# Performance work log

Measured on AMD Instinct MI355X. Metric: run time of the kernel, lower is better.

## Reference

```python
import jax, jax.numpy as jnp
import numpy as np

B, S, K_IN = 8, 2048, 512
D_MODEL = 1024
N_INPUT = 2048
N_PROCESS = 4096
HIDDEN = 4096  # default hidden_dim = n_input * 2
K = 256


def setup_inputs() -> dict:
    key = jax.random.key(0)
    ks = jax.random.split(key, 7)
    return {
        "selected_activations": jax.random.normal(ks[0], (B, S, K_IN), dtype=jnp.float32),
        "selected_indices": jax.random.randint(ks[1], (B, K_IN), 0, N_INPUT),
        "k": K,
        "combination_weights": jax.random.normal(ks[2], (N_PROCESS, N_INPUT), dtype=jnp.float32) * np.float32(np.sqrt(2.0 / N_INPUT)),
        "output_projections": jax.random.normal(ks[3], (N_PROCESS, D_MODEL), dtype=jnp.float32) * np.float32(np.sqrt(2.0 / N_PROCESS)),
        "w1": jax.random.normal(ks[4], (HIDDEN, N_INPUT), dtype=jnp.float32) * np.float32(np.sqrt(2.0 / (N_INPUT + HIDDEN))),
        "b1": jnp.zeros((HIDDEN,), dtype=jnp.float32),
        "w2": jax.random.normal(ks[5], (N_PROCESS, HIDDEN), dtype=jnp.float32) * np.float32(np.sqrt(2.0 / (HIDDEN + N_PROCESS))),
        "b2": jnp.zeros((N_PROCESS,), dtype=jnp.float32),
    }


def reference(selected_activations, selected_indices, k, combination_weights,
              output_projections, w1, b1, w2, b2):
    bsz = selected_indices.shape[0]
    n_input = combination_weights.shape[1]

    # Per-batch gather of combination weights: [B, k_in, n_process]
    sel_w = combination_weights.T[selected_indices]

    # Process activations: [B, S, n_process], exact (erf) GELU like torch F.gelu
    process_activations = jax.nn.gelu(
        jnp.einsum('bsk,bkp->bsp', selected_activations, sel_w), approximate=False)

    # One-hot style input-selection mask via scatter: [B, n_input]
    input_selection = jnp.zeros((bsz, n_input), dtype=jnp.float32)
    input_selection = input_selection.at[jnp.arange(bsz)[:, None], selected_indices].set(1.0)

    # Combination analyzer MLP: Linear -> GELU -> Linear
    h = jax.nn.gelu(input_selection @ w1.T + b1, approximate=False)
    combination_relevance = h @ w2.T + b2  # [B, n_process]

    # Router scores and top-k process selection
    activation_scores = process_activations.max(axis=1)  # [B, n_process]
    final_scores = activation_scores * jax.nn.sigmoid(combination_relevance)
    _, process_indices = jax.lax.top_k(final_scores, k)  # [B, k]

    # Gather selected process activations [B, S, k] and projections [B, k, d_model]
    sel_pa = jnp.take_along_axis(process_activations, process_indices[:, None, :], axis=2)
    sel_proj = output_projections[process_indices]

    # Final projection: [B, S, d_model]
    return jnp.einsum('bsk,bkd->bsd', sel_pa, sel_proj)
```

## Files before the change

### kernel.cpp

```cpp
#include <hip/hip_runtime.h>
#include <math.h>

#define B 8
#define S 2048
#define KIN 512
#define NIN 2048
#define NP 4096
#define HID 4096
#define DM 1024
#define TOPK 256

typedef __bf16 bf16x8 __attribute__((ext_vector_type(8)));
typedef __bf16 bf16x4 __attribute__((ext_vector_type(4)));
typedef float f32x4 __attribute__((ext_vector_type(4)));

__device__ __forceinline__ float gelu_exact(float x) {
    return 0.5f * x * (1.0f + erff(x * 0.70710678118654752440f));
}

__device__ __forceinline__ void atomicMaxFloat(float* addr, float val) {
    if (val >= 0.0f) atomicMax((int*)addr, __float_as_int(val));
    else             atomicMin((unsigned int*)addr, __float_as_uint(val));
}

__device__ __forceinline__ void async_copy16(void* lds, const void* g) {
    __builtin_amdgcn_global_load_lds(
        (__attribute__((address_space(1))) void*)g,
        (__attribute__((address_space(3))) void*)lds, 16, 0, 0);
}

__global__ __launch_bounds__(256) void init_kernel(float* scores, float* relacc,
                                                   float* hacc, unsigned* maskb,
                                                   int* selcnt) {
    int t = blockIdx.x * blockDim.x + threadIdx.x;
    if (t < B * NP)  { scores[t] = __int_as_float(0xFF800000); relacc[t] = 0.f; }
    if (t < B * HID) hacc[t] = 0.f;
    if (t < NIN)     maskb[t] = 0u;
    if (t < B)       selcnt[t] = 0;
}

__global__ __launch_bounds__(256) void scatter_maskbits(const int* __restrict__ idx,
                                                        unsigned* __restrict__ maskb) {
    int t = blockIdx.x * blockDim.x + threadIdx.x;
    if (t >= B * KIN) return;
    int b = t / KIN;
    atomicOr(&maskb[idx[t]], 1u << b);
}

__global__ __launch_bounds__(256) void pack_A(const float* __restrict__ A,
                                              __bf16* __restrict__ Apack) {
    size_t t = (size_t)blockIdx.x * 256 + threadIdx.x;
    size_t f = t * 4;
    size_t rowi = f >> 9;
    int j = (int)(f & 511);
    float4 v = *(const float4*)(A + f);
    __bf16 h0 = (__bf16)v.x, h1 = (__bf16)v.y, h2 = (__bf16)v.z, h3 = (__bf16)v.w;
    bf16x4 hv = {h0, h1, h2, h3};
    bf16x4 lv = {(__bf16)(v.x - (float)h0), (__bf16)(v.y - (float)h1),
                 (__bf16)(v.z - (float)h2), (__bf16)(v.w - (float)h3)};
    __bf16* orow = Apack + rowi * 1024;
    *(bf16x4*)(orow + j) = hv;
    *(bf16x4*)(orow + 512 + j) = lv;
}

__global__ __launch_bounds__(256) void gather_pack_w(const float* __restrict__ cw,
                                                     const int* __restrict__ idx,
                                                     __bf16* __restrict__ wpack) {
    __shared__ float rowbuf[4][NIN];
    __shared__ int sidx[B][KIN];
    int p0 = blockIdx.x * 4;
    int tid = threadIdx.x;
    for (int t = tid; t < B * KIN; t += 256) sidx[t >> 9][t & 511] = idx[t];
#pragma unroll
    for (int r = 0; r < 4; ++r)
        for (int c = tid; c < NIN / 4; c += 256)
            *(float4*)&rowbuf[r][c * 4] = *(const float4*)&cw[(size_t)(p0 + r) * NIN + c * 4];
    __syncthreads();
#pragma unroll
    for (int r = 0; r < 4; ++r) {
        int p = p0 + r;
        for (int b = 0; b < B; ++b) {
            __bf16* orow = wpack + ((size_t)b * NP + p) * 1024;
            for (int j = tid; j < KIN; j += 256) {
                float x = rowbuf[r][sidx[b][j]];
                __bf16 hh = (__bf16)x;
                orow[j] = hh;
                orow[512 + j] = (__bf16)(x - (float)hh);
            }
        }
    }
}

template <int EPI, int NSEG, int KSEG, int LDA, int LDB, int BROWS, int LDOUT>
__global__ __launch_bounds__(256) void mfma_gemm(const __bf16* __restrict__ Ap,
                                                 const __bf16* __restrict__ Bp,
                                                 void* __restrict__ outp) {
    __shared__ __align__(16) __bf16 As[128 * 64];
    __shared__ __align__(16) __bf16 Ws[128 * 64];
    const int b = blockIdx.z;
    const int s0 = blockIdx.x * 128;
    const int p0 = blockIdx.y * 128;
    const int tid = threadIdx.x;
    const int w = tid >> 6, lane = tid & 63;
    const int wr = w >> 1, wc = w & 1;
    const int ldRow = lane >> 3;
    const int ldCol = ((lane & 7) ^ (ldRow & 7)) * 8;
    const int fr = lane & 15;
    const int fq = lane >> 4;
    const __bf16* Ab = Ap + ((size_t)b * S + s0) * LDA;
    const __bf16* Bb = Bp + ((size_t)b * BROWS + p0) * LDB;

    f32x4 acc[4][4] = {};

    for (int seg = 0; seg < NSEG; ++seg) {
        const int aoff = (seg == 1) ? KSEG : 0;
        const int boff = (seg == 2) ? KSEG : 0;
        for (int k0 = 0; k0 < KSEG; k0 += 64) {
            __syncthreads();
#pragma unroll
            for (int i = 0; i < 4; ++i) {
                const __bf16* g = Ab + (size_t)(w * 32 + i * 8 + ldRow) * LDA + aoff + k0 + ldCol;
                async_copy16(&As[(w * 32 + i * 8) * 64], g);
            }
#pragma unroll
            for (int i = 0; i < 4; ++i) {
                const __bf16* g = Bb + (size_t)(w * 32 + i * 8 + ldRow) * LDB + boff + k0 + ldCol;
                async_copy16(&Ws[(w * 32 + i * 8) * 64], g);
            }
            __syncthreads();
#pragma unroll
            for (int ks = 0; ks < 2; ++ks) {
                bf16x8 af[4], bfr[4];
#pragma unroll
                for (int i = 0; i < 4; ++i) {
                    int R = wr * 64 + i * 16 + fr;
                    af[i] = *(const bf16x8*)&As[R * 64 + (((ks * 4 + fq) ^ (R & 7)) * 8)];
                }
#pragma unroll
                for (int j = 0; j < 4; ++j) {
                    int R = wc * 64 + j * 16 + fr;
                    bfr[j] = *(const bf16x8*)&Ws[R * 64 + (((ks * 4 + fq) ^ (R & 7)) * 8)];
                }
#pragma unroll
                for (int i = 0; i < 4; ++i)
#pragma unroll
                    for (int j = 0; j < 4; ++j)
                        acc[i][j] = __builtin_amdgcn_mfma_f32_16x16x32_bf16(af[i], bfr[j], acc[i][j], 0, 0, 0);
            }
        }
    }

    if constexpr (EPI == 1) {
        __bf16* o = (__bf16*)outp;
#pragma unroll
        for (int i = 0; i < 4; ++i)
#pragma unroll
            for (int r = 0; r < 4; ++r) {
                size_t row = (size_t)b * S + s0 + wr * 64 + i * 16 + fq * 4 + r;
#pragma unroll
                for (int j = 0; j < 4; ++j)
                    o[row * LDOUT + p0 + wc * 64 + j * 16 + fr] = (__bf16)gelu_exact(acc[i][j][r]);
            }
    } else {
        float* o = (float*)outp;
#pragma unroll
        for (int i = 0; i < 4; ++i)
#pragma unroll
            for (int r = 0; r < 4; ++r) {
                size_t row = (size_t)b * S + s0 + wr * 64 + i * 16 + fq * 4 + r;
#pragma unroll
                for (int j = 0; j < 4; ++j)
                    o[row * LDOUT + p0 + wc * 64 + j * 16 + fr] = acc[i][j][r];
            }
    }
}

__device__ __forceinline__ void stage64(__bf16* ldsTile, const __bf16* gRow0,
                                        int rbase, int ldg, int koff, int w, int lane) {
    const int rr = lane >> 3;
    const int gc = ((lane & 7) ^ rr) * 8;
    const __bf16* g = gRow0 + (size_t)(rbase + w * 8 + rr) * ldg + (koff + gc);
    async_copy16(ldsTile + (rbase + w * 8) * 64, g);
}

template <int EPI, int NSEG, int KSEG, int LDA, int LDB, int BROWS, int LDOUT>
__global__ __launch_bounds__(512, 2) void mfma_gemm256(const __bf16* __restrict__ Ap,
                                                       const __bf16* __restrict__ Bp,
                                                       void* __restrict__ outp) {
    constexpr int TPS = KSEG / 64;
    constexpr int NT = NSEG * TPS;
    __shared__ __align__(16) __bf16 As[2][256 * 64];
    __shared__ __align__(16) __bf16 Ws[2][256 * 64];

    const int flat = blockIdx.x + (blockIdx.y << 3) + (blockIdx.z << 7);
    const int b = flat & 7;
    const int j = flat >> 3;
    const int s0 = (j & 7) * 256;
    const int p0 = (j >> 3) * 256;

    const int tid = threadIdx.x;
    const int w = tid >> 6, lane = tid & 63;
    const int wr = w >> 2, wc = w & 3;
    const int fr = lane & 15, fq = lane >> 4;
    const __bf16* Ab = Ap + ((size_t)b * S + s0) * LDA;
    const __bf16* Bb = Bp + ((size_t)b * BROWS + p0) * LDB;

    auto offs = [&](int t, int& ao, int& bo) {
        int seg = t / TPS, k0 = (t % TPS) * 64;
        ao = ((NSEG == 3 && seg == 1) ? KSEG : 0) + k0;
        bo = ((NSEG == 3 && seg == 2) ? KSEG : 0) + k0;
    };

    int offA[2][2][4];
    int offB[2][4];
#pragma unroll
    for (int kk = 0; kk < 2; ++kk) {
#pragma unroll
        for (int mh = 0; mh < 2; ++mh)
#pragma unroll
            for (int mi = 0; mi < 4; ++mi) {
                int R = wr * 128 + mh * 64 + mi * 16 + fr;
                offA[kk][mh][mi] = R * 64 + (((kk * 4 + fq) ^ (R & 7)) * 8);
            }
#pragma unroll
        for (int nj = 0; nj < 4; ++nj) {
            int R = wc * 64 + nj * 16 + fr;
            offB[kk][nj] = R * 64 + (((kk * 4 + fq) ^ (R & 7)) * 8);
        }
    }

    f32x4 acc[8][4] = {};

    {
        int ao, bo;
        offs(0, ao, bo);
        stage64(&As[0][0], Ab, 0, LDA, ao, w, lane);
        stage64(&As[0][0], Ab, 128, LDA, ao, w, lane);
        stage64(&As[0][0], Ab, 64, LDA, ao, w, lane);
        stage64(&As[0][0], Ab, 192, LDA, ao, w, lane);
        stage64(&Ws[0][0], Bb, 0, LDB, bo, w, lane);
        stage64(&Ws[0][0], Bb, 128, LDB, bo, w, lane);
        stage64(&Ws[0][0], Bb, 64, LDB, bo, w, lane);
        stage64(&Ws[0][0], Bb, 192, LDB, bo, w, lane);
        if (NT > 1) {
            offs(1, ao, bo);
            stage64(&As[1][0], Ab, 0, LDA, ao, w, lane);
            stage64(&As[1][0], Ab, 128, LDA, ao, w, lane);
            stage64(&Ws[1][0], Bb, 0, LDB, bo, w, lane);
            stage64(&Ws[1][0], Bb, 128, LDB, bo, w, lane);
            asm volatile("s_waitcnt vmcnt(4)");
        } else {
            asm volatile("s_waitcnt vmcnt(0)");
        }
        __builtin_amdgcn_s_barrier();
    }

    for (int t = 0; t < NT; ++t) {
        const __bf16* Asb = &As[t & 1][0];
        const __bf16* Wsb = &Ws[t & 1][0];
        __bf16* Asn = &As[(t & 1) ^ 1][0];
        __bf16* Wsn = &Ws[(t & 1) ^ 1][0];
        bf16x8 af[4], bfr[4];

#pragma unroll
        for (int i = 0; i < 4; ++i) af[i] = *(const bf16x8*)&Asb[offA[0][0][i]];
#pragma unroll
        for (int n = 0; n < 4; ++n) bfr[n] = *(const bf16x8*)&Wsb[offB[0][n]];
        if (t + 1 < NT) {
            int ao, bo;
            offs(t + 1, ao, bo);
            stage64(Asn, Ab, 64, LDA, ao, w, lane);
            stage64(Asn, Ab, 192, LDA, ao, w, lane);
            stage64(Wsn, Bb, 64, LDB, bo, w, lane);
            stage64(Wsn, Bb, 192, LDB, bo, w, lane);
        }
        __builtin_amdgcn_s_barrier();
        asm volatile("s_waitcnt lgkmcnt(0)");
        __builtin_amdgcn_s_setprio(1);
#pragma unroll
        for (int mi = 0; mi < 4; ++mi)
#pragma unroll
            for (int nj = 0; nj < 4; ++nj)
                acc[mi][nj] = __builtin_amdgcn_mfma_f32_16x16x32_bf16(af[mi], bfr[nj], acc[mi][nj], 0, 0, 0);
        __builtin_amdgcn_s_setprio(0);
        __builtin_amdgcn_s_barrier();

#pragma unroll
        for (int i = 0; i < 4; ++i) af[i] = *(const bf16x8*)&Asb[offA[0][1][i]];
        __builtin_amdgcn_s_barrier();
        asm volatile("s_waitcnt lgkmcnt(0)");
        __builtin_amdgcn_s_setprio(1);
#pragma unroll
        for (int mi = 0; mi < 4; ++mi)
#pragma unroll
            for (int nj = 0; nj < 4; ++nj)
                acc[4 + mi][nj] = __builtin_amdgcn_mfma_f32_16x16x32_bf16(af[mi], bfr[nj], acc[4 + mi][nj], 0, 0, 0);
        __builtin_amdgcn_s_setprio(0);
        __builtin_amdgcn_s_barrier();

#pragma unroll
        for (int i = 0; i < 4; ++i) af[i] = *(const bf16x8*)&Asb[offA[1][0][i]];
#pragma unroll
        for (int n = 0; n < 4; ++n) bfr[n] = *(const bf16x8*)&Wsb[offB[1][n]];
        __builtin_amdgcn_s_barrier();
        asm volatile("s_waitcnt lgkmcnt(0)");
        __builtin_amdgcn_s_setprio(1);
#pragma unroll
        for (int mi = 0; mi < 4; ++mi)
#pragma unroll
            for (int nj = 0; nj < 4; ++nj)
                acc[mi][nj] = __builtin_amdgcn_mfma_f32_16x16x32_bf16(af[mi], bfr[nj], acc[mi][nj], 0, 0, 0);
        __builtin_amdgcn_s_setprio(0);
        __builtin_amdgcn_s_barrier();

#pragma unroll
        for (int i = 0; i < 4; ++i) af[i] = *(const bf16x8*)&Asb[offA[1][1][i]];
        if (t + 2 < NT) {
            int ao, bo;
            offs(t + 2, ao, bo);
            stage64((__bf16*)Asb, Ab, 0, LDA, ao, w, lane);
            stage64((__bf16*)Asb, Ab, 128, LDA, ao, w, lane);
            stage64((__bf16*)Wsb, Bb, 0, LDB, bo, w, lane);
            stage64((__bf16*)Wsb, Bb, 128, LDB, bo, w, lane);
            asm volatile("s_waitcnt vmcnt(4)");
        } else {
            asm volatile("s_waitcnt vmcnt(0)");
        }
        __builtin_amdgcn_s_barrier();
        asm volatile("s_waitcnt lgkmcnt(0)");
        __builtin_amdgcn_s_setprio(1);
#pragma unroll
        for (int mi = 0; mi < 4; ++mi)
#pragma unroll
            for (int nj = 0; nj < 4; ++nj)
                acc[4 + mi][nj] = __builtin_amdgcn_mfma_f32_16x16x32_bf16(af[mi], bfr[nj], acc[4 + mi][nj], 0, 0, 0);
        __builtin_amdgcn_s_setprio(0);
        __builtin_amdgcn_s_barrier();
    }

    if constexpr (EPI == 0) {
        float* scores = (float*)outp;
#pragma unroll
        for (int nj = 0; nj < 4; ++nj) {
            float mx = -INFINITY, mn = INFINITY;
#pragma unroll
            for (int mi = 0; mi < 8; ++mi)
#pragma unroll
                for (int r = 0; r < 4; ++r) {
                    float v = acc[mi][nj][r];
                    mx = fmaxf(mx, v);
                    mn = fminf(mn, v);
                }
            mx = fmaxf(mx, __shfl_xor(mx, 16));
            mx = fmaxf(mx, __shfl_xor(mx, 32));
            mn = fminf(mn, __shfl_xor(mn, 16));
            mn = fminf(mn, __shfl_xor(mn, 32));
            if (fq == 0) {
                float m = fmaxf(gelu_exact(mx), gelu_exact(mn));
                atomicMaxFloat(&scores[(size_t)b * LDOUT + p0 + wc * 64 + nj * 16 + fr], m);
            }
        }
    } else if constexpr (EPI == 1) {
        __bf16* o = (__bf16*)outp;
#pragma unroll
        for (int mi = 0; mi < 8; ++mi)
#pragma unroll
            for (int r = 0; r < 4; ++r) {
                size_t row = (size_t)b * S + s0 + wr * 128 + mi * 16 + fq * 4 + r;
#pragma unroll
                for (int nj = 0; nj < 4; ++nj)
                    o[row * LDOUT + p0 + wc * 64 + nj * 16 + fr] = (__bf16)gelu_exact(acc[mi][nj][r]);
            }
    } else {
        float* o = (float*)outp;
#pragma unroll
        for (int mi = 0; mi < 8; ++mi)
#pragma unroll
            for (int r = 0; r < 4; ++r) {
                size_t row = (size_t)b * S + s0 + wr * 128 + mi * 16 + fq * 4 + r;
#pragma unroll
                for (int nj = 0; nj < 4; ++nj)
                    o[row * LDOUT + p0 + wc * 64 + nj * 16 + fr] = acc[mi][nj][r];
            }
    }
}

__global__ __launch_bounds__(256) void mlp1_part(const float* __restrict__ w1,
                                                 const unsigned* __restrict__ maskb,
                                                 float* __restrict__ hacc) {
    __shared__ unsigned smb[512];
    int i0 = blockIdx.x * 64;
    int c0 = blockIdx.y * 512;
    int tid = threadIdx.x;
    for (int c = tid; c < 512; c += 256) smb[c] = maskb[c0 + c];
    __syncthreads();
    int r = tid >> 2, cq = tid & 3;
    const float* row = w1 + (size_t)(i0 + r) * NIN + c0;
    float acc[B] = {};
    for (int it = 0; it < 32; ++it) {
        int c = it * 16 + cq * 4;
        float4 v = *(const float4*)(row + c);
        float vv[4] = {v.x, v.y, v.z, v.w};
#pragma unroll
        for (int e = 0; e < 4; ++e) {
            unsigned mb = smb[c + e];
#pragma unroll
            for (int bb = 0; bb < B; ++bb)
                if (mb & (1u << bb)) acc[bb] += vv[e];
        }
    }
#pragma unroll
    for (int bb = 0; bb < B; ++bb)
        atomicAdd(&hacc[bb * HID + i0 + r], acc[bb]);
}

__global__ __launch_bounds__(256) void fin1(const float* __restrict__ hacc,
                                            const float* __restrict__ b1,
                                            float* __restrict__ h) {
    int t = blockIdx.x * 256 + threadIdx.x;
    if (t < B * HID) h[t] = gelu_exact(hacc[t] + b1[t & (HID - 1)]);
}

__global__ __launch_bounds__(256) void mlp2_part(const float* __restrict__ w2,
                                                 const float* __restrict__ h,
                                                 float* __restrict__ relacc) {
    __shared__ float sh[B][512];
    int p0 = blockIdx.x * 64;
    int c0 = blockIdx.y * 512;
    int tid = threadIdx.x;
    for (int i = tid; i < B * 128; i += 256) {
        int bb = i >> 7, c4 = i & 127;
        *(float4*)&sh[bb][c4 * 4] = *(const float4*)&h[(size_t)bb * HID + c0 + c4 * 4];
    }
    __syncthreads();
    int r = tid >> 2, cq = tid & 3;
    const float* row = w2 + (size_t)(p0 + r) * HID + c0;
    float acc[B] = {};
    for (int it = 0; it < 32; ++it) {
        int c = it * 16 + cq * 4;
        float4 v = *(const float4*)(row + c);
#pragma unroll
        for (int bb = 0; bb < B; ++bb)
            acc[bb] += v.x * sh[bb][c] + v.y * sh[bb][c + 1] + v.z * sh[bb][c + 2] + v.w * sh[bb][c + 3];
    }
#pragma unroll
    for (int bb = 0; bb < B; ++bb)
        atomicAdd(&relacc[bb * NP + p0 + r], acc[bb]);
}

__global__ __launch_bounds__(256) void topk_select(const float* __restrict__ scores,
                                                   const float* __restrict__ relacc,
                                                   const float* __restrict__ b2,
                                                   int* __restrict__ selidx,
                                                   int* __restrict__ selcnt) {
    __shared__ float sc[NP];
    int b = blockIdx.y;
    int p = blockIdx.x * 256 + threadIdx.x;
    for (int c = threadIdx.x; c < NP; c += 256) {
        float rel = relacc[(size_t)b * NP + c] + b2[c];
        sc[c] = scores[(size_t)b * NP + c] * (1.0f / (1.0f + expf(-rel)));
    }
    __syncthreads();
    float my = sc[p];
    int cnt = 0;
    for (int q = 0; q < NP; ++q) {
        float v = sc[q];
        cnt += (v > my) || (v == my && q < p);
    }
    if (cnt < TOPK) {
        int pos = atomicAdd(&selcnt[b], 1);
        selidx[b * TOPK + pos] = p;
    }
}

__global__ __launch_bounds__(256) void wsel_gather(const __bf16* __restrict__ wpack,
                                                   const int* __restrict__ selidx,
                                                   __bf16* __restrict__ wsel) {
    int kk = blockIdx.x, b = blockIdx.y;
    int sel = selidx[b * TOPK + kk];
    const unsigned* src = (const unsigned*)(wpack + ((size_t)b * NP + sel) * 1024);
    unsigned* dst = (unsigned*)(wsel + ((size_t)b * TOPK + kk) * 512);
    dst[threadIdx.x] = src[threadIdx.x];
}

__global__ __launch_bounds__(256) void projT_gather(const float* __restrict__ proj,
                                                    const int* __restrict__ selidx,
                                                    __bf16* __restrict__ PT) {
    __shared__ float tile[64][68];
    __shared__ int sel[64];
    int b = blockIdx.z, d0 = blockIdx.x * 64, k0 = blockIdx.y * 64;
    int tid = threadIdx.x;
    if (tid < 64) sel[tid] = selidx[b * TOPK + k0 + tid];
    __syncthreads();
    for (int r = 0; r < 4; ++r) {
        int kk = r * 16 + (tid >> 4);
        float4 v = *(const float4*)&proj[(size_t)sel[kk] * DM + d0 + (tid & 15) * 4];
        *(float4*)&tile[kk][(tid & 15) * 4] = v;
    }
    __syncthreads();
    for (int r = 0; r < 16; ++r) {
        int dd = r * 4 + (tid >> 6);
        int kk = tid & 63;
        PT[((size_t)b * DM + d0 + dd) * TOPK + k0 + kk] = (__bf16)tile[kk][dd];
    }
}

extern "C" void kernel_launch(void* const* d_in, const int* in_sizes, int n_in,
                              void* d_out, int out_size, void* d_ws, size_t ws_size,
                              hipStream_t stream) {
    const float* A    = (const float*)d_in[0];
    const int*   idx  = (const int*)d_in[1];
    const float* cw   = (const float*)d_in[3];
    const float* proj = (const float*)d_in[4];
    const float* w1   = (const float*)d_in[5];
    const float* b1   = (const float*)d_in[6];
    const float* w2   = (const float*)d_in[7];
    const float* b2   = (const float*)d_in[8];
    float* out = (float*)d_out;

    char* ws = (char*)d_ws;
    size_t off = 0;
    auto alloc = [&](size_t bytes) {
        void* p = ws + off;
        off += (bytes + 255) & ~(size_t)255;
        return p;
    };
    __bf16* Apack = (__bf16*)alloc((size_t)B * S * 1024 * 2);
    __bf16* Wpack = (__bf16*)alloc((size_t)B * NP * 1024 * 2);
    __bf16* selpa = (__bf16*)alloc((size_t)B * S * TOPK * 2);
    __bf16* PT    = (__bf16*)alloc((size_t)B * DM * TOPK * 2);
    __bf16* Wsel  = (__bf16*)alloc((size_t)B * TOPK * 512 * 2);
    float* scores = (float*)alloc((size_t)B * NP * 4);
    float* relacc = (float*)alloc((size_t)B * NP * 4);
    float* hacc   = (float*)alloc((size_t)B * HID * 4);
    float* h      = (float*)alloc((size_t)B * HID * 4);
    unsigned* maskb = (unsigned*)alloc((size_t)NIN * 4);
    int* selidx   = (int*)alloc((size_t)B * TOPK * 4);
    int* selcnt   = (int*)alloc((size_t)B * 4);

    init_kernel<<<dim3((B * HID + 255) / 256), 256, 0, stream>>>(scores, relacc, hacc, maskb, selcnt);
    scatter_maskbits<<<dim3((B * KIN + 255) / 256), 256, 0, stream>>>(idx, maskb);
    pack_A<<<dim3((B * S * KIN / 4) / 256), 256, 0, stream>>>(A, Apack);
    gather_pack_w<<<dim3(NP / 4), 256, 0, stream>>>(cw, idx, Wpack);

    mfma_gemm256<0, 3, 512, 1024, 1024, NP, NP>
        <<<dim3(S / 256, NP / 256, B), 512, 0, stream>>>(Apack, Wpack, (void*)scores);

    mlp1_part<<<dim3(HID / 64, NIN / 512), 256, 0, stream>>>(w1, maskb, hacc);
    fin1<<<dim3((B * HID + 255) / 256), 256, 0, stream>>>(hacc, b1, h);
    mlp2_part<<<dim3(NP / 64, HID / 512), 256, 0, stream>>>(w2, h, relacc);

    topk_select<<<dim3(NP / 256, B), 256, 0, stream>>>(scores, relacc, b2, selidx, selcnt);

    wsel_gather<<<dim3(TOPK, B), 256, 0, stream>>>(Wpack, selidx, Wsel);
    projT_gather<<<dim3(DM / 64, TOPK / 64, B), 256, 0, stream>>>(proj, selidx, PT);

    mfma_gemm<1, 1, 512, 1024, 512, TOPK, TOPK>
        <<<dim3(S / 128, TOPK / 128, B), 256, 0, stream>>>(Apack, Wsel, (void*)selpa);

    mfma_gemm<2, 1, 256, 256, 256, DM, DM>
        <<<dim3(S / 128, DM / 128, B), 256, 0, stream>>>(selpa, PT, (void*)out);
}
```

Before: 672.7 us.

## Double-buffer MFMA register fragments to overlap LDS reads with matrix ops

Restructures the GEMM main loop so LDS fragment loads for the next quarter-step go into alternate register sets (rA0/rA1, rB0/rB1) while the current MFMA block runs. It prefetches the next tile's first fragments at the end of each iteration, adds sched_barriers and memory clobbers to fix instruction order, and cuts one barrier per quarter. The aim is to hide LDS latency behind MFMA issue. In exchange it uses more VGPRs and moves the vmcnt waits, including a full vmcnt(0) in mid-iteration, which could stall on global loads or hurt occupancy.

```diff
diff --git a/kernel.cpp b/kernel.cpp
--- a/kernel.cpp
+++ b/kernel.cpp
@@ -229,7 +229,24 @@
         }
     }
 
+    bf16x8 rA0[4], rA1[4], rB0[4], rB1[4];
     f32x4 acc[8][4] = {};
+
+    auto RDA = [&](bf16x8* dst, const __bf16* base, int mh, int kk) {
+#pragma unroll
+        for (int i = 0; i < 4; ++i) dst[i] = *(const bf16x8*)&base[offA[kk][mh][i]];
+    };
+    auto RDB = [&](bf16x8* dst, const __bf16* base, int kk) {
+#pragma unroll
+        for (int n = 0; n < 4; ++n) dst[n] = *(const bf16x8*)&base[offB[kk][n]];
+    };
+    auto MMA = [&](int q, const bf16x8* a, const bf16x8* bf) {
+#pragma unroll
+        for (int mi = 0; mi < 4; ++mi)
+#pragma unroll
+            for (int nj = 0; nj < 4; ++nj)
+                acc[q + mi][nj] = __builtin_amdgcn_mfma_f32_16x16x32_bf16(a[mi], bf[nj], acc[q + mi][nj], 0, 0, 0);
+    };
 
     {
         int ao, bo;
@@ -248,94 +265,77 @@
             stage64(&As[1][0], Ab, 128, LDA, ao, w, lane);
             stage64(&Ws[1][0], Bb, 0, LDB, bo, w, lane);
             stage64(&Ws[1][0], Bb, 128, LDB, bo, w, lane);
-            asm volatile("s_waitcnt vmcnt(4)");
+            asm volatile("s_waitcnt vmcnt(4)" ::: "memory");
         } else {
-            asm volatile("s_waitcnt vmcnt(0)");
+            asm volatile("s_waitcnt vmcnt(0)" ::: "memory");
         }
         __builtin_amdgcn_s_barrier();
+        RDA(rA0, &As[0][0], 0, 0);
+        RDB(rB0, &Ws[0][0], 0);
     }
 
     for (int t = 0; t < NT; ++t) {
-        const __bf16* Asb = &As[t & 1][0];
-        const __bf16* Wsb = &Ws[t & 1][0];
-        __bf16* Asn = &As[(t & 1) ^ 1][0];
-        __bf16* Wsn = &Ws[(t & 1) ^ 1][0];
-        bf16x8 af[4], bfr[4];
-
-#pragma unroll
-        for (int i = 0; i < 4; ++i) af[i] = *(const bf16x8*)&Asb[offA[0][0][i]];
-#pragma unroll
-        for (int n = 0; n < 4; ++n) bfr[n] = *(const bf16x8*)&Wsb[offB[0][n]];
+        const int cur = t & 1, nxt = cur ^ 1;
+        const __bf16* Asb = &As[cur][0];
+        const __bf16* Wsb = &Ws[cur][0];
+
+        __builtin_amdgcn_s_barrier();
+        asm volatile("s_waitcnt lgkmcnt(0)" ::: "memory");
+        __builtin_amdgcn_sched_barrier(0);
+        __builtin_amdgcn_s_setprio(1);
+        MMA(0, rA0, rB0);
+        __builtin_amdgcn_s_setprio(0);
+        __builtin_amdgcn_sched_barrier(0);
         if (t + 1 < NT) {
             int ao, bo;
             offs(t + 1, ao, bo);
-            stage64(Asn, Ab, 64, LDA, ao, w, lane);
-            stage64(Asn, Ab, 192, LDA, ao, w, lane);
-            stage64(Wsn, Bb, 64, LDB, bo, w, lane);
-            stage64(Wsn, Bb, 192, LDB, bo, w, lane);
-        }
+            stage64(&As[nxt][0], Ab, 64, LDA, ao, w, lane);
+            stage64(&As[nxt][0], Ab, 192, LDA, ao, w, lane);
+            stage64(&Ws[nxt][0], Bb, 64, LDB, bo, w, lane);
+            stage64(&Ws[nxt][0], Bb, 192, LDB, bo, w, lane);
+        }
+        RDA(rA1, Asb, 1, 0);
+
         __builtin_amdgcn_s_barrier();
-        asm volatile("s_waitcnt lgkmcnt(0)");
+        asm volatile("s_waitcnt lgkmcnt(0)" ::: "memory");
+        __builtin_amdgcn_sched_barrier(0);
         __builtin_amdgcn_s_setprio(1);
-#pragma unroll
-        for (int mi = 0; mi < 4; ++mi)
-#pragma unroll
-            for (int nj = 0; nj < 4; ++nj)
-                acc[mi][nj] = __builtin_amdgcn_mfma_f32_16x16x32_bf16(af[mi], bfr[nj], acc[mi][nj], 0, 0, 0);
+        MMA(4, rA1, rB0);
         __builtin_amdgcn_s_setprio(0);
+        __builtin_amdgcn_sched_barrier(0);
+        RDA(rA0, Asb, 0, 1);
+        RDB(rB1, Wsb, 1);
+
         __builtin_amdgcn_s_barrier();
-
-#pragma unroll
-        for (int i = 0; i < 4; ++i) af[i] = *(const bf16x8*)&Asb[offA[0][1][i]];
+        asm volatile("s_waitcnt lgkmcnt(0)" ::: "memory");
+        __builtin_amdgcn_sched_barrier(0);
+        __builtin_amdgcn_s_setprio(1);
+        MMA(0, rA0, rB1);
+        __builtin_amdgcn_s_setprio(0);
+        __builtin_amdgcn_sched_barrier(0);
+        asm volatile("s_waitcnt vmcnt(0)" ::: "memory");
+        __builtin_amdgcn_sched_barrier(0);
+        RDA(rA1, Asb, 1, 1);
+
         __builtin_amdgcn_s_barrier();
-        asm volatile("s_waitcnt lgkmcnt(0)");
+        asm volatile("s_waitcnt lgkmcnt(0)" ::: "memory");
+        __builtin_amdgcn_sched_barrier(0);
         __builtin_amdgcn_s_setprio(1);
-#pragma unroll
-        for (int mi = 0; mi < 4; ++mi)
-#pragma unroll
-            for (int nj = 0; nj < 4; ++nj)
-                acc[4 + mi][nj] = __builtin_amdgcn_mfma_f32_16x16x32_bf16(af[mi], bfr[nj], acc[4 + mi][nj], 0, 0, 0);
+        MMA(4, rA1, rB1);
         __builtin_amdgcn_s_setprio(0);
-        __builtin_amdgcn_s_barrier();
-
-#pragma unroll
-        for (int i = 0; i < 4; ++i) af[i] = *(const bf16x8*)&Asb[offA[1][0][i]];
-#pragma unroll
-        for (int n = 0; n < 4; ++n) bfr[n] = *(const bf16x8*)&Wsb[offB[1][n]];
-        __builtin_amdgcn_s_barrier();
-        asm volatile("s_waitcnt lgkmcnt(0)");
-        __builtin_amdgcn_s_setprio(1);
-#pragma unroll
-        for (int mi = 0; mi < 4; ++mi)
-#pragma unroll
-            for (int nj = 0; nj < 4; ++nj)
-                acc[mi][nj] = __builtin_amdgcn_mfma_f32_16x16x32_bf16(af[mi], bfr[nj], acc[mi][nj], 0, 0, 0);
-        __builtin_amdgcn_s_setprio(0);
-        __builtin_amdgcn_s_barrier();
-
-#pragma unroll
-        for (int i = 0; i < 4; ++i) af[i] = *(const bf16x8*)&Asb[offA[1][1][i]];
+        __builtin_amdgcn_sched_barrier(0);
         if (t + 2 < NT) {
             int ao, bo;
             offs(t + 2, ao, bo);
-            stage64((__bf16*)Asb, Ab, 0, LDA, ao, w, lane);
-            stage64((__bf16*)Asb, Ab, 128, LDA, ao, w, lane);
-            stage64((__bf16*)Wsb, Bb, 0, LDB, bo, w, lane);
-            stage64((__bf16*)Wsb, Bb, 128, LDB, bo, w, lane);
-            asm volatile("s_waitcnt vmcnt(4)");
-        } else {
-            asm volatile("s_waitcnt vmcnt(0)");
-        }
-        __builtin_amdgcn_s_barrier();
-        asm volatile("s_waitcnt lgkmcnt(0)");
-        __builtin_amdgcn_s_setprio(1);
-#pragma unroll
-        for (int mi = 0; mi < 4; ++mi)
-#pragma unroll
-            for (int nj = 0; nj < 4; ++nj)
-                acc[4 + mi][nj] = __builtin_amdgcn_mfma_f32_16x16x32_bf16(af[mi], bfr[nj], acc[4 + mi][nj], 0, 0, 0);
-        __builtin_amdgcn_s_setprio(0);
-        __builtin_amdgcn_s_barrier();
+            stage64(&As[cur][0], Ab, 0, LDA, ao, w, lane);
+            stage64(&As[cur][0], Ab, 128, LDA, ao, w, lane);
+            stage64(&Ws[cur][0], Bb, 0, LDB, bo, w, lane);
+            stage64(&Ws[cur][0], Bb, 128, LDB, bo, w, lane);
+        }
+        if (t + 1 < NT) {
+            RDA(rA0, &As[nxt][0], 0, 0);
+            RDB(rB0, &Ws[nxt][0], 0);
+        }
     }
 
     if constexpr (EPI == 0) {
```

Result: slower. 698.6 us (+3.9%).
